# Optimization experiments

Hardware: AMD Instinct MI355X
Metric: run time of the kernel (lower is better)

The kernel has to match this reference:

```python
import jax, jax.numpy as jnp
import numpy as np

B, T, D, H, E, K = 4, 2048, 1024, 2048, 8, 2
LN_EPS = 1e-5


def setup_inputs() -> dict:
    key = jax.random.key(0)
    ks = jax.random.split(key, 5)
    sc = 0.02  # init scale for weights
    return {
        "x": jax.random.normal(ks[0], (B, T, D), dtype=jnp.float32),
        "gate_W": jax.random.normal(ks[1], (D, E), dtype=jnp.float32) * sc,
        "gate_b": jnp.zeros((E,), dtype=jnp.float32),
        "W1": jax.random.normal(ks[2], (E, D, H), dtype=jnp.float32) * sc,
        "b1": jnp.zeros((E, H), dtype=jnp.float32),
        "W2": jax.random.normal(ks[3], (E, H, D), dtype=jnp.float32) * sc,
        "b2": jnp.zeros((E, D), dtype=jnp.float32),
        "ln_gamma": jnp.ones((D,), dtype=jnp.float32),
        "ln_beta": jnp.zeros((D,), dtype=jnp.float32),
    }


def reference(x, gate_W, gate_b, W1, b1, W2, b2, ln_gamma, ln_beta):
    b, t, d = x.shape
    tokens = x.reshape(b * t, d)                      # [N, D]
    n = tokens.shape[0]

    # --- noisy top-k router (eval mode: no noise) ---
    logits = tokens @ gate_W + gate_b                 # [N, E]
    topk_val, topk_idx = jax.lax.top_k(logits, K)     # [N, K]
    topk_prob = jax.nn.softmax(topk_val, axis=-1)
    gates = jnp.zeros_like(logits).at[jnp.arange(n)[:, None], topk_idx].set(topk_prob)  # [N, E]

    # --- experts: dense-equivalent of gather-MLP-scatter (gates are 0 for unselected) ---
    h = jax.nn.gelu(jnp.einsum('nd,edh->enh', tokens, W1) + b1[:, None, :], approximate=False)  # [E,N,H]
    y = jnp.einsum('enh,ehd->end', h, W2) + b2[:, None, :]                                      # [E,N,D]
    out = jnp.einsum('ne,end->nd', gates, y).reshape(b, t, d)

    # --- residual + layernorm ---
    z = out + x
    mu = jnp.mean(z, axis=-1, keepdims=True)
    var = jnp.var(z, axis=-1, keepdims=True)
    out = (z - mu) * jax.lax.rsqrt(var + LN_EPS) * ln_gamma + ln_beta

    # --- aux losses ---
    route_probs = jax.nn.softmax(logits, axis=-1)     # [N, E]
    importance = route_probs.mean(axis=0)             # [E]
    load = (gates > 0).astype(jnp.float32).mean(axis=0)  # [E]
    balance_loss = E * jnp.sum(importance * load)
    eps = 1e-8
    entropy = -(route_probs * jnp.log(route_probs + eps)).sum(axis=-1).mean()
    utilization_entropy = -(load * jnp.log(load + eps)).sum()
    return out, balance_loss, entropy, utilization_entropy, load, importance
```

## Files before the change

### kernel.cpp

```cpp
#include <hip/hip_runtime.h>
#include <math.h>

#define N_TOK 8192
#define DIM   1024
#define HID   2048
#define NE    8
#define NPAIR (N_TOK * 2)
#define CAPP  (NPAIR + NE * 128)
#define TAIL  (N_TOK * DIM)

typedef __bf16 bf16x8_t __attribute__((ext_vector_type(8)));
typedef float  f32x4_t  __attribute__((ext_vector_type(4)));

__device__ __forceinline__ unsigned short f2bf(float f) {
  union { float f; unsigned u; } v; v.f = f;
  unsigned r = v.u + 0x7fffu + ((v.u >> 16) & 1u);
  return (unsigned short)(r >> 16);
}

__device__ __forceinline__ float bf2f(unsigned short h) {
  union { unsigned u; float f; } v; v.u = ((unsigned)h) << 16;
  return v.f;
}

__device__ __forceinline__ float gelu_exact(float v) {
  return 0.5f * v * (1.f + erff(v * 0.70710678118654752440f));
}

__device__ __forceinline__ void load16_lds(const void* g, void* l) {
  __builtin_amdgcn_global_load_lds(
      (const __attribute__((address_space(1))) unsigned int*)g,
      (__attribute__((address_space(3))) unsigned int*)l, 16, 0, 0);
}


template<int KD, int RR>
__device__ __forceinline__ void w2f_body(const float* __restrict__ src,
                                         unsigned short* __restrict__ dst,
                                         int bx, int kblk, int z,
                                         unsigned short (*L)[34], int t) {
  constexpr int KD32 = KD / 32;
  int r0 = bx << 8;
  const float* s = src + (size_t)z * KD * RR + (size_t)(kblk * 32) * RR + r0 + t;
  #pragma unroll
  for (int kk = 0; kk < 32; ++kk)
    L[t][kk] = f2bf(s[(size_t)kk * RR]);
  __syncthreads();
  int lane = t & 63, m16 = lane & 15, q = lane >> 4;
  unsigned short* d = dst + (size_t)z * KD * RR;
  #pragma unroll
  for (int p = 0; p < 4; ++p) {
    int ci = p * 4 + (t >> 6);
    int c = ((r0 >> 4) + ci) * KD32 + kblk;
    uint4 v = *(const uint4*)&L[ci * 16 + m16][q * 8];
    *(uint4*)(d + (size_t)c * 512 + lane * 8) = v;
  }
}

__global__ __launch_bounds__(256) void w_to_frag_all(
    const float* __restrict__ W1, const float* __restrict__ W2,
    unsigned short* __restrict__ W1f, unsigned short* __restrict__ W2f,
    float* __restrict__ stats) {
  __shared__ unsigned short L[256][34];
  int t = threadIdx.x;
  int f = blockIdx.x;
  if (f == 0 && t < 64) stats[t] = 0.f;
  if (f < 2048) {
    int z = f >> 8, r = f & 255;
    w2f_body<DIM, HID>(W1, W1f, r & 7, r >> 3, z, L, t);
  } else {
    int f2 = f - 2048;
    int z = f2 >> 8, r = f2 & 255;
    w2f_body<HID, DIM>(W2, W2f, r & 3, r >> 2, z, L, t);
  }
}

#define R_BLOCKS 512
#define R_TPW    (N_TOK / (R_BLOCKS * 4))
__global__ __launch_bounds__(256) void router_kernel(
    const float* __restrict__ x, const float* __restrict__ gW, const float* __restrict__ gb,
    int* __restrict__ tok_e, float* __restrict__ tok_g,
    int* __restrict__ cnt, float* __restrict__ imp, float* __restrict__ ent_sum) {
  __shared__ int s_cnt[NE];
  __shared__ float s_imp[NE];
  __shared__ float s_ent;
  int tid = threadIdx.x;
  if (tid < NE) { s_cnt[tid] = 0; s_imp[tid] = 0.f; }
  if (tid == 0) s_ent = 0.f;
  __syncthreads();
  int wid = tid >> 6, lane = tid & 63;
  int t0 = (blockIdx.x * 4 + wid) * R_TPW;
  float imp_loc[8] = {0.f, 0.f, 0.f, 0.f, 0.f, 0.f, 0.f, 0.f};
  float ent_loc = 0.f;
  for (int t = 0; t < R_TPW; ++t) {
    int n = t0 + t;
    const float* xr = x + (size_t)n * DIM;
    float p[8] = {0.f, 0.f, 0.f, 0.f, 0.f, 0.f, 0.f, 0.f};
    #pragma unroll
    for (int it = 0; it < DIM / 64; ++it) {
      int d = lane + (it << 6);
      float xv = xr[d];
      const float4* g4 = (const float4*)(gW + (size_t)d * NE);
      float4 a = g4[0], b = g4[1];
      p[0] += xv * a.x; p[1] += xv * a.y; p[2] += xv * a.z; p[3] += xv * a.w;
      p[4] += xv * b.x; p[5] += xv * b.y; p[6] += xv * b.z; p[7] += xv * b.w;
    }
    #pragma unroll
    for (int e = 0; e < 8; ++e)
      for (int o = 32; o > 0; o >>= 1) p[e] += __shfl_down(p[e], o, 64);
    if (lane == 0) {
      float lg[8];
      #pragma unroll
      for (int e = 0; e < 8; ++e) lg[e] = p[e] + gb[e];
      int i0 = 0;
      #pragma unroll
      for (int e = 1; e < 8; ++e) if (lg[e] > lg[i0]) i0 = e;
      int i1 = (i0 == 0) ? 1 : 0;
      #pragma unroll
      for (int e = 0; e < 8; ++e) if (e != i0 && lg[e] > lg[i1]) i1 = e;
      float d1 = expf(lg[i1] - lg[i0]);
      float g0 = 1.f / (1.f + d1);
      float g1 = d1 * g0;
      tok_e[2 * n] = i0; tok_e[2 * n + 1] = i1;
      tok_g[2 * n] = g0; tok_g[2 * n + 1] = g1;
      atomicAdd(&s_cnt[i0], 1);
      atomicAdd(&s_cnt[i1], 1);
      float mx = lg[i0], s = 0.f, pe[8];
      #pragma unroll
      for (int e = 0; e < 8; ++e) { pe[e] = expf(lg[e] - mx); s += pe[e]; }
      float inv = 1.f / s;
      #pragma unroll
      for (int e = 0; e < 8; ++e) {
        float pr = pe[e] * inv;
        imp_loc[e] += pr;
        ent_loc -= pr * logf(pr + 1e-8f);
      }
    }
  }
  if (lane == 0) {
    #pragma unroll
    for (int e = 0; e < 8; ++e) atomicAdd(&s_imp[e], imp_loc[e]);
    atomicAdd(&s_ent, ent_loc);
  }
  __syncthreads();
  const float invN = 1.f / (float)N_TOK;
  if (tid < NE) {
    atomicAdd(&cnt[tid], s_cnt[tid]);
    atomicAdd(&imp[tid], s_imp[tid] * invN);
  }
  if (tid == NE) atomicAdd(ent_sum, s_ent * invN);
}

__global__ __launch_bounds__(256) void scatter_kernel(
    const int* __restrict__ tok_e, const float* __restrict__ tok_g,
    const int* __restrict__ cnt, const float* __restrict__ imp,
    const float* __restrict__ ent_sum,
    int* __restrict__ cursor, int* __restrict__ poffs_g, float* __restrict__ out_tail,
    int* __restrict__ row_token, float* __restrict__ row_gate,
    int* __restrict__ pair_slot) {
  __shared__ int s_cnt[NE], s_base[NE], s_rank[NE];
  int tid = threadIdx.x;
  if (tid < NE) { s_cnt[tid] = 0; s_rank[tid] = 0; }
  __syncthreads();
  int n = blockIdx.x * 256 + tid;
  int e0 = tok_e[2 * n], e1 = tok_e[2 * n + 1];
  atomicAdd(&s_cnt[e0], 1);
  atomicAdd(&s_cnt[e1], 1);
  __syncthreads();
  if (tid < NE) {
    int po = 0;
    for (int e = 0; e < tid; ++e) po += ((cnt[e] + 127) >> 7) << 7;
    s_base[tid] = po + atomicAdd(&cursor[tid], s_cnt[tid]);
  }
  __syncthreads();
  int r0 = atomicAdd(&s_rank[e0], 1);
  int s0 = s_base[e0] + r0;
  row_token[s0] = n; row_gate[s0] = tok_g[2 * n]; pair_slot[2 * n] = s0;
  int r1 = atomicAdd(&s_rank[e1], 1);
  int s1 = s_base[e1] + r1;
  row_token[s1] = n; row_gate[s1] = tok_g[2 * n + 1]; pair_slot[2 * n + 1] = s1;
  if (blockIdx.x == 0 && tid == 0) {
    int off = 0; float bal = 0.f, util = 0.f;
    for (int e = 0; e < NE; ++e) {
      poffs_g[e] = off;
      off += ((cnt[e] + 127) >> 7) << 7;
      float ld = (float)cnt[e] * (1.f / (float)N_TOK);
      float im = imp[e];
      out_tail[3 + e] = ld;
      out_tail[11 + e] = im;
      bal += im * ld;
      util -= ld * logf(ld + 1e-8f);
    }
    poffs_g[NE] = off;
    out_tail[0] = (float)NE * bal;
    out_tail[1] = *ent_sum;
    out_tail[2] = util;
  }
}

#define GA_BLOCKS ((CAPP >> 4) * 32 / 4)
__global__ __launch_bounds__(256) void gather_a1(
    const float* __restrict__ x, const int* __restrict__ row_token,
    const int* __restrict__ cnt, const int* __restrict__ poffs,
    unsigned short* __restrict__ Ab1) {
  int po[NE + 1];
  #pragma unroll
  for (int i = 0; i <= NE; ++i) po[i] = poffs[i];
  int nch = (po[NE] >> 4) * 32;
  int cl = blockIdx.x * 4 + (threadIdx.x >> 6);
  if (cl >= nch) return;
  int lane = threadIdx.x & 63, m16 = lane & 15, q = lane >> 4;
  int sb = cl >> 5, kblk = cl & 31;
  int slot = (sb << 4) + m16;
  int e = 0;
  #pragma unroll
  for (int k = 1; k < NE; ++k) e += (po[k] <= slot) ? 1 : 0;
  int sl = slot - po[e];
  int tok = (sl < cnt[e]) ? row_token[slot] : 0;
  int k = kblk * 32 + q * 8;
  const float4* sp = (const float4*)(x + (size_t)tok * DIM + k);
  float4 v0 = sp[0], v1 = sp[1];
  unsigned short t[8] = {f2bf(v0.x), f2bf(v0.y), f2bf(v0.z), f2bf(v0.w),
                         f2bf(v1.x), f2bf(v1.y), f2bf(v1.z), f2bf(v1.w)};
  *(uint4*)(Ab1 + ((size_t)sb * 32 + kblk) * 512 + lane * 8) = *(uint4*)t;
}

#define GEMM_BLOCKS 1024

__device__ __forceinline__ int xcd_swz(int bid) {
  return (bid & 7) * (GEMM_BLOCKS >> 3) + (bid >> 3);
}

__global__ __launch_bounds__(256, 4) void expert_gemm1(
    const unsigned short* __restrict__ Ab1,
    const unsigned short* __restrict__ W1f,
    const float* __restrict__ b1,
    const int* __restrict__ poffs,
    unsigned short* __restrict__ He) {
  __shared__ __align__(16) unsigned short As[8192], Bs[8192];
  __shared__ int s_po[NE + 1];
  int tid = threadIdx.x, wid = tid >> 6, lane = tid & 63;
  if (tid <= NE) s_po[tid] = poffs[tid];
  __syncthreads();
  int nt = (s_po[NE] >> 7) << 4;
  int m16 = lane & 15, q = lane >> 4;
  int wr = (wid & 1) << 6, wc = (wid >> 1) << 6;
  int ra = wr >> 4, rc = wc >> 4;
  unsigned short* lA = As + wid * 4 * 512;
  unsigned short* lB = Bs + wid * 4 * 512;
  f32x4_t zero4 = {0.f, 0.f, 0.f, 0.f};
  int bid0 = xcd_swz(blockIdx.x);

  for (int tile = bid0; tile < nt; tile += GEMM_BLOCKS) {
    int rt = tile >> 4, ct = tile & 15;
    int col0 = ct << 7;
    int row0 = rt << 7;
    int e = 0;
    while (e + 1 < NE && s_po[e + 1] <= row0) ++e;
    const unsigned short* Ag = Ab1 + ((size_t)((rt << 3) + wid * 2) * 32) * 512 + lane * 8;
    const unsigned short* Bg = W1f + (size_t)e * HID * DIM
                             + ((size_t)((col0 >> 4) + wid * 2) * 32) * 512 + lane * 8;
    f32x4_t acc[4][4];
    #pragma unroll
    for (int i = 0; i < 4; ++i)
      #pragma unroll
      for (int j = 0; j < 4; ++j) acc[i][j] = zero4;

    for (int k0 = 0; k0 < DIM; k0 += 64) {
      int kc = (k0 >> 5) * 512;
      load16_lds(Ag + kc,                  lA);
      load16_lds(Ag + kc + 512,            lA + 512);
      load16_lds(Ag + kc + 32 * 512,       lA + 1024);
      load16_lds(Ag + kc + 32 * 512 + 512, lA + 1536);
      load16_lds(Bg + kc,                  lB);
      load16_lds(Bg + kc + 512,            lB + 512);
      load16_lds(Bg + kc + 32 * 512,       lB + 1024);
      load16_lds(Bg + kc + 32 * 512 + 512, lB + 1536);
      __syncthreads();
      #pragma unroll
      for (int ks = 0; ks < 2; ++ks) {
        bf16x8_t a[4], b[4];
        #pragma unroll
        for (int i = 0; i < 4; ++i) {
          a[i] = *(const bf16x8_t*)&As[((ra + i) * 2 + ks) * 512 + lane * 8];
          b[i] = *(const bf16x8_t*)&Bs[((rc + i) * 2 + ks) * 512 + lane * 8];
        }
        #pragma unroll
        for (int i = 0; i < 4; ++i)
          #pragma unroll
          for (int j = 0; j < 4; ++j)
            acc[i][j] = __builtin_amdgcn_mfma_f32_16x16x32_bf16(a[i], b[j], acc[i][j], 0, 0, 0);
      }
      __syncthreads();
    }

    const float* b1e = b1 + (size_t)e * HID;
    int sb = rt << 3;
    #pragma unroll
    for (int i = 0; i < 4; ++i) {
      size_t sblk = (size_t)(sb + ra + i);
      #pragma unroll
      for (int rr = 0; rr < 4; ++rr) {
        int s15 = q * 4 + rr;
        #pragma unroll
        for (int j = 0; j < 4; ++j) {
          int col = col0 + wc + j * 16 + m16;
          float v = acc[i][j][rr] + b1e[col];
          size_t off = (sblk * 64 + (col >> 5)) * 512 + (((col >> 3) & 3) * 16 + s15) * 8 + (col & 7);
          He[off] = f2bf(gelu_exact(v));
        }
      }
    }
  }
}

__global__ __launch_bounds__(256, 4) void expert_gemm2(
    const unsigned short* __restrict__ He,
    const unsigned short* __restrict__ W2f,
    const int* __restrict__ poffs,
    unsigned short* __restrict__ yb) {
  __shared__ __align__(16) unsigned short As[8192], Bs[8192];
  __shared__ int s_po[NE + 1];
  int tid = threadIdx.x, wid = tid >> 6, lane = tid & 63;
  if (tid <= NE) s_po[tid] = poffs[tid];
  __syncthreads();
  int nt = (s_po[NE] >> 7) << 3;
  int m16 = lane & 15, q = lane >> 4;
  int wr = (wid & 1) << 6, wc = (wid >> 1) << 6;
  int ra = wr >> 4, rc = wc >> 4;
  unsigned short* lA = As + wid * 4 * 512;
  unsigned short* lB = Bs + wid * 4 * 512;
  f32x4_t zero4 = {0.f, 0.f, 0.f, 0.f};
  int bid0 = xcd_swz(blockIdx.x);

  for (int tile = bid0; tile < nt; tile += GEMM_BLOCKS) {
    int rt = tile >> 3, ct = tile & 7;
    int row0 = rt << 7;
    int col0 = ct << 7;
    int e = 0;
    while (e + 1 < NE && s_po[e + 1] <= row0) ++e;
    const unsigned short* Ag = He + ((size_t)((rt << 3) + wid * 2) * 64) * 512 + lane * 8;
    const unsigned short* Bg = W2f + (size_t)e * DIM * HID
                             + ((size_t)((col0 >> 4) + wid * 2) * 64) * 512 + lane * 8;
    f32x4_t acc[4][4];
    #pragma unroll
    for (int i = 0; i < 4; ++i)
      #pragma unroll
      for (int j = 0; j < 4; ++j) acc[i][j] = zero4;

    for (int k0 = 0; k0 < HID; k0 += 64) {
      int kc = (k0 >> 5) * 512;
      load16_lds(Ag + kc,                  lA);
      load16_lds(Ag + kc + 512,            lA + 512);
      load16_lds(Ag + kc + 64 * 512,       lA + 1024);
      load16_lds(Ag + kc + 64 * 512 + 512, lA + 1536);
      load16_lds(Bg + kc,                  lB);
      load16_lds(Bg + kc + 512,            lB + 512);
      load16_lds(Bg + kc + 64 * 512,       lB + 1024);
      load16_lds(Bg + kc + 64 * 512 + 512, lB + 1536);
      __syncthreads();
      #pragma unroll
      for (int ks = 0; ks < 2; ++ks) {
        bf16x8_t a[4], b[4];
        #pragma unroll
        for (int i = 0; i < 4; ++i) {
          a[i] = *(const bf16x8_t*)&As[((ra + i) * 2 + ks) * 512 + lane * 8];
          b[i] = *(const bf16x8_t*)&Bs[((rc + i) * 2 + ks) * 512 + lane * 8];
        }
        #pragma unroll
        for (int i = 0; i < 4; ++i)
          #pragma unroll
          for (int j = 0; j < 4; ++j)
            acc[i][j] = __builtin_amdgcn_mfma_f32_16x16x32_bf16(a[i], b[j], acc[i][j], 0, 0, 0);
      }
      __syncthreads();
    }

    #pragma unroll
    for (int i = 0; i < 4; ++i) {
      #pragma unroll
      for (int rr = 0; rr < 4; ++rr) {
        size_t slot = (size_t)(row0 + wr + i * 16 + q * 4 + rr);
        #pragma unroll
        for (int j = 0; j < 4; ++j) {
          int col = col0 + wc + j * 16 + m16;
          yb[slot * DIM + col] = f2bf(acc[i][j][rr]);
        }
      }
    }
  }
}

__global__ __launch_bounds__(256) void ln_kernel(
    const float* __restrict__ x, const unsigned short* __restrict__ yb,
    const int* __restrict__ tok_e, const float* __restrict__ tok_g,
    const int* __restrict__ pair_slot, const float* __restrict__ b2,
    const float* __restrict__ gamma, const float* __restrict__ beta,
    float* __restrict__ out) {
  int n = blockIdx.x, tid = threadIdx.x;
  int e0 = tok_e[2 * n], e1 = tok_e[2 * n + 1];
  float g0 = tok_g[2 * n], g1 = tok_g[2 * n + 1];
  size_t s0 = (size_t)pair_slot[2 * n], s1 = (size_t)pair_slot[2 * n + 1];
  const float* xr = x + (size_t)n * DIM;
  const unsigned short* y0 = yb + s0 * DIM;
  const unsigned short* y1 = yb + s1 * DIM;
  const float* b2e0 = b2 + (size_t)e0 * DIM;
  const float* b2e1 = b2 + (size_t)e1 * DIM;
  int d0 = tid << 2;
  float4 xv  = *(const float4*)(xr + d0);
  ushort4 yv0 = *(const ushort4*)(y0 + d0);
  ushort4 yv1 = *(const ushort4*)(y1 + d0);
  float4 bv0 = *(const float4*)(b2e0 + d0);
  float4 bv1 = *(const float4*)(b2e1 + d0);
  float z[4], s = 0.f, s2 = 0.f;
  {
    const float* xp = (const float*)&xv;
    const unsigned short* y0p = (const unsigned short*)&yv0;
    const unsigned short* y1p = (const unsigned short*)&yv1;
    const float* b0p = (const float*)&bv0;
    const float* b1p = (const float*)&bv1;
    #pragma unroll
    for (int jj = 0; jj < 4; ++jj) {
      float v = xp[jj] + g0 * (bf2f(y0p[jj]) + b0p[jj]) + g1 * (bf2f(y1p[jj]) + b1p[jj]);
      z[jj] = v; s += v; s2 += v * v;
    }
  }
  for (int o = 32; o > 0; o >>= 1) { s += __shfl_down(s, o, 64); s2 += __shfl_down(s2, o, 64); }
  __shared__ float rs[4], rs2[4];
  int wid = tid >> 6, lane = tid & 63;
  if (lane == 0) { rs[wid] = s; rs2[wid] = s2; }
  __syncthreads();
  float ts = rs[0] + rs[1] + rs[2] + rs[3];
  float ts2 = rs2[0] + rs2[1] + rs2[2] + rs2[3];
  float mu = ts * (1.f / DIM);
  float var = ts2 * (1.f / DIM) - mu * mu;
  float rstd = rsqrtf(var + 1e-5f);
  float4 gv = *(const float4*)(gamma + d0);
  float4 bv = *(const float4*)(beta + d0);
  float4 ov;
  {
    const float* gp = (const float*)&gv;
    const float* bp = (const float*)&bv;
    float* op = (float*)&ov;
    #pragma unroll
    for (int jj = 0; jj < 4; ++jj)
      op[jj] = (z[jj] - mu) * rstd * gp[jj] + bp[jj];
  }
  *(float4*)(out + (size_t)n * DIM + d0) = ov;
}

extern "C" void kernel_launch(void* const* d_in, const int* in_sizes, int n_in,
                              void* d_out, int out_size, void* d_ws, size_t ws_size,
                              hipStream_t stream) {
  const float* x     = (const float*)d_in[0];
  const float* gW    = (const float*)d_in[1];
  const float* gb    = (const float*)d_in[2];
  const float* W1    = (const float*)d_in[3];
  const float* b1    = (const float*)d_in[4];
  const float* W2    = (const float*)d_in[5];
  const float* b2    = (const float*)d_in[6];
  const float* gamma = (const float*)d_in[7];
  const float* beta  = (const float*)d_in[8];
  float* out = (float*)d_out;

  char* w = (char*)d_ws;
  unsigned short* W1f = (unsigned short*)w; w += (size_t)NE * HID * DIM * 2;
  unsigned short* W2f = (unsigned short*)w; w += (size_t)NE * DIM * HID * 2;
  unsigned short* He  = (unsigned short*)w; w += (size_t)CAPP * HID * 2;
  unsigned short* AbY = (unsigned short*)w; w += (size_t)CAPP * DIM * 2;
  int*   row_token    = (int*)w;            w += (size_t)CAPP * 4;
  float* row_gate     = (float*)w;          w += (size_t)CAPP * 4;
  int*   tok_e        = (int*)w;            w += (size_t)NPAIR * 4;
  float* tok_g        = (float*)w;          w += (size_t)NPAIR * 4;
  int*   pair_slot    = (int*)w;            w += (size_t)NPAIR * 4;
  float* imp          = (float*)w;
  float* ent_sum      = imp + 8;
  int*   cntp         = (int*)(imp + 16);
  int*   cursor       = cntp + 8;
  int*   poffs        = cursor + 8;

  unsigned short* Ab1 = AbY;
  unsigned short* yb  = AbY;

  w_to_frag_all<<<4096, 256, 0, stream>>>(W1, W2, W1f, W2f, imp);
  router_kernel<<<R_BLOCKS, 256, 0, stream>>>(x, gW, gb, tok_e, tok_g, cntp, imp, ent_sum);
  scatter_kernel<<<N_TOK / 256, 256, 0, stream>>>(tok_e, tok_g, cntp, imp, ent_sum,
                                                  cursor, poffs, out + TAIL,
                                                  row_token, row_gate, pair_slot);
  gather_a1<<<GA_BLOCKS, 256, 0, stream>>>(x, row_token, cntp, poffs, Ab1);
  expert_gemm1<<<GEMM_BLOCKS, 256, 0, stream>>>(Ab1, W1f, b1, poffs, He);
  expert_gemm2<<<GEMM_BLOCKS, 256, 0, stream>>>(He, W2f, poffs, yb);
  ln_kernel<<<N_TOK, 256, 0, stream>>>(x, yb, tok_e, tok_g, pair_slot, b2, gamma, beta, out);
}
```

Before: 451.6 us.

## Fuse router into weight-prep kernel and use contiguous tile ranges in GEMMs

Merges the weight-to-fragment conversion and the router into one launch, so router blocks run alongside the weight conversion blocks and one kernel launch is dropped. Global atomics for counts, importance and entropy are replaced by per-block partials that each scatter block reduces itself, which removes the need to zero stats before the router. Both expert GEMMs now give each block a contiguous range of tiles (assuming 1024 blocks) instead of a strided loop, which improves locality of shared weight columns and rows. Costs include a redundant partial reduction in every scatter block and possible load imbalance from the range split.

```diff
diff --git a/kernel.cpp b/kernel.cpp
--- a/kernel.cpp
+++ b/kernel.cpp
@@ -33,6 +33,10 @@
       (__attribute__((address_space(3))) unsigned int*)l, 16, 0, 0);
 }
 
+
+#define W2F_BLOCKS 4096
+#define R_BLOCKS   512
+#define R_TPW      (N_TOK / (R_BLOCKS * 4))
 
 template<int KD, int RR>
 __device__ __forceinline__ void w2f_body(const float* __restrict__ src,
@@ -57,43 +61,43 @@
   }
 }
 
-__global__ __launch_bounds__(256) void w_to_frag_all(
+__global__ __launch_bounds__(256) void prep_kernel(
     const float* __restrict__ W1, const float* __restrict__ W2,
     unsigned short* __restrict__ W1f, unsigned short* __restrict__ W2f,
-    float* __restrict__ stats) {
+    const float* __restrict__ x, const float* __restrict__ gW, const float* __restrict__ gb,
+    int* __restrict__ tok_e, float* __restrict__ tok_g,
+    int* __restrict__ pcnt,
+    float* __restrict__ pimp,
+    float* __restrict__ pent,
+    int* __restrict__ cursor) {
   __shared__ unsigned short L[256][34];
+  __shared__ int s_cnt[NE];
+  __shared__ float s_imp[NE];
+  __shared__ float s_ent;
   int t = threadIdx.x;
   int f = blockIdx.x;
-  if (f == 0 && t < 64) stats[t] = 0.f;
   if (f < 2048) {
     int z = f >> 8, r = f & 255;
     w2f_body<DIM, HID>(W1, W1f, r & 7, r >> 3, z, L, t);
-  } else {
+    return;
+  }
+  if (f < W2F_BLOCKS) {
     int f2 = f - 2048;
     int z = f2 >> 8, r = f2 & 255;
     w2f_body<HID, DIM>(W2, W2f, r & 3, r >> 2, z, L, t);
-  }
-}
-
-#define R_BLOCKS 512
-#define R_TPW    (N_TOK / (R_BLOCKS * 4))
-__global__ __launch_bounds__(256) void router_kernel(
-    const float* __restrict__ x, const float* __restrict__ gW, const float* __restrict__ gb,
-    int* __restrict__ tok_e, float* __restrict__ tok_g,
-    int* __restrict__ cnt, float* __restrict__ imp, float* __restrict__ ent_sum) {
-  __shared__ int s_cnt[NE];
-  __shared__ float s_imp[NE];
-  __shared__ float s_ent;
-  int tid = threadIdx.x;
-  if (tid < NE) { s_cnt[tid] = 0; s_imp[tid] = 0.f; }
-  if (tid == 0) s_ent = 0.f;
-  __syncthreads();
-  int wid = tid >> 6, lane = tid & 63;
-  int t0 = (blockIdx.x * 4 + wid) * R_TPW;
+    return;
+  }
+  int rb = f - W2F_BLOCKS;
+  if (rb == 0 && t < NE) cursor[t] = 0;
+  if (t < NE) { s_cnt[t] = 0; s_imp[t] = 0.f; }
+  if (t == 0) s_ent = 0.f;
+  __syncthreads();
+  int wid = t >> 6, lane = t & 63;
+  int t0 = (rb * 4 + wid) * R_TPW;
   float imp_loc[8] = {0.f, 0.f, 0.f, 0.f, 0.f, 0.f, 0.f, 0.f};
   float ent_loc = 0.f;
-  for (int t = 0; t < R_TPW; ++t) {
-    int n = t0 + t;
+  for (int tt = 0; tt < R_TPW; ++tt) {
+    int n = t0 + tt;
     const float* xr = x + (size_t)n * DIM;
     float p[8] = {0.f, 0.f, 0.f, 0.f, 0.f, 0.f, 0.f, 0.f};
     #pragma unroll
@@ -143,25 +147,41 @@
     atomicAdd(&s_ent, ent_loc);
   }
   __syncthreads();
-  const float invN = 1.f / (float)N_TOK;
-  if (tid < NE) {
-    atomicAdd(&cnt[tid], s_cnt[tid]);
-    atomicAdd(&imp[tid], s_imp[tid] * invN);
-  }
-  if (tid == NE) atomicAdd(ent_sum, s_ent * invN);
+  if (t < NE) { pcnt[rb * NE + t] = s_cnt[t]; pimp[rb * NE + t] = s_imp[t]; }
+  if (t == NE) pent[rb] = s_ent;
 }
 
 __global__ __launch_bounds__(256) void scatter_kernel(
     const int* __restrict__ tok_e, const float* __restrict__ tok_g,
-    const int* __restrict__ cnt, const float* __restrict__ imp,
-    const float* __restrict__ ent_sum,
-    int* __restrict__ cursor, int* __restrict__ poffs_g, float* __restrict__ out_tail,
+    const int* __restrict__ pcnt, const float* __restrict__ pimp,
+    const float* __restrict__ pent,
+    int* __restrict__ cursor, int* __restrict__ poffs_g, int* __restrict__ cnt_out,
+    float* __restrict__ out_tail,
     int* __restrict__ row_token, float* __restrict__ row_gate,
     int* __restrict__ pair_slot) {
   __shared__ int s_cnt[NE], s_base[NE], s_rank[NE];
+  __shared__ int g_cnt[NE];
+  __shared__ float g_imp[NE], g_ent;
   int tid = threadIdx.x;
-  if (tid < NE) { s_cnt[tid] = 0; s_rank[tid] = 0; }
-  __syncthreads();
+  if (tid < NE) { s_cnt[tid] = 0; s_rank[tid] = 0; g_cnt[tid] = 0; g_imp[tid] = 0.f; }
+  if (tid == 0) g_ent = 0.f;
+  __syncthreads();
+  {
+    int e = tid & 7, rg = tid >> 3;
+    int acc = 0;
+    #pragma unroll
+    for (int r = 0; r < 16; ++r) acc += pcnt[(rg * 16 + r) * NE + e];
+    atomicAdd(&g_cnt[e], acc);
+  }
+  if (blockIdx.x == 0) {
+    int e = tid & 7, rg = tid >> 3;
+    float fa = 0.f;
+    #pragma unroll
+    for (int r = 0; r < 16; ++r) fa += pimp[(rg * 16 + r) * NE + e];
+    atomicAdd(&g_imp[e], fa);
+    float ea = pent[tid] + pent[tid + 256];
+    atomicAdd(&g_ent, ea);
+  }
   int n = blockIdx.x * 256 + tid;
   int e0 = tok_e[2 * n], e1 = tok_e[2 * n + 1];
   atomicAdd(&s_cnt[e0], 1);
@@ -169,7 +189,7 @@
   __syncthreads();
   if (tid < NE) {
     int po = 0;
-    for (int e = 0; e < tid; ++e) po += ((cnt[e] + 127) >> 7) << 7;
+    for (int e = 0; e < tid; ++e) po += ((g_cnt[e] + 127) >> 7) << 7;
     s_base[tid] = po + atomicAdd(&cursor[tid], s_cnt[tid]);
   }
   __syncthreads();
@@ -180,12 +200,14 @@
   int s1 = s_base[e1] + r1;
   row_token[s1] = n; row_gate[s1] = tok_g[2 * n + 1]; pair_slot[2 * n + 1] = s1;
   if (blockIdx.x == 0 && tid == 0) {
+    const float invN = 1.f / (float)N_TOK;
     int off = 0; float bal = 0.f, util = 0.f;
     for (int e = 0; e < NE; ++e) {
       poffs_g[e] = off;
-      off += ((cnt[e] + 127) >> 7) << 7;
-      float ld = (float)cnt[e] * (1.f / (float)N_TOK);
-      float im = imp[e];
+      cnt_out[e] = g_cnt[e];
+      off += ((g_cnt[e] + 127) >> 7) << 7;
+      float ld = (float)g_cnt[e] * invN;
+      float im = g_imp[e] * invN;
       out_tail[3 + e] = ld;
       out_tail[11 + e] = im;
       bal += im * ld;
@@ -193,7 +215,7 @@
     }
     poffs_g[NE] = off;
     out_tail[0] = (float)NE * bal;
-    out_tail[1] = *ent_sum;
+    out_tail[1] = g_ent * invN;
     out_tail[2] = util;
   }
 }
@@ -249,9 +271,11 @@
   unsigned short* lA = As + wid * 4 * 512;
   unsigned short* lB = Bs + wid * 4 * 512;
   f32x4_t zero4 = {0.f, 0.f, 0.f, 0.f};
-  int bid0 = xcd_swz(blockIdx.x);
-
-  for (int tile = bid0; tile < nt; tile += GEMM_BLOCKS) {
+  int swz = xcd_swz(blockIdx.x);
+  int lo = (int)(((long long)swz * nt) >> 10);
+  int hi = (int)(((long long)(swz + 1) * nt) >> 10);
+
+  for (int tile = lo; tile < hi; ++tile) {
     int rt = tile >> 4, ct = tile & 15;
     int col0 = ct << 7;
     int row0 = rt << 7;
@@ -331,9 +355,11 @@
   unsigned short* lA = As + wid * 4 * 512;
   unsigned short* lB = Bs + wid * 4 * 512;
   f32x4_t zero4 = {0.f, 0.f, 0.f, 0.f};
-  int bid0 = xcd_swz(blockIdx.x);
-
-  for (int tile = bid0; tile < nt; tile += GEMM_BLOCKS) {
+  int swz = xcd_swz(blockIdx.x);
+  int lo = (int)(((long long)swz * nt) >> 10);
+  int hi = (int)(((long long)(swz + 1) * nt) >> 10);
+
+  for (int tile = lo; tile < hi; ++tile) {
     int rt = tile >> 3, ct = tile & 7;
     int row0 = rt << 7;
     int col0 = ct << 7;
@@ -473,21 +499,22 @@
   int*   tok_e        = (int*)w;            w += (size_t)NPAIR * 4;
   float* tok_g        = (float*)w;          w += (size_t)NPAIR * 4;
   int*   pair_slot    = (int*)w;            w += (size_t)NPAIR * 4;
-  float* imp          = (float*)w;
-  float* ent_sum      = imp + 8;
-  int*   cntp         = (int*)(imp + 16);
-  int*   cursor       = cntp + 8;
-  int*   poffs        = cursor + 8;
+  int*   cursor       = (int*)w;            w += 64;
+  int*   poffs        = (int*)w;            w += 64;
+  int*   cnt_out      = (int*)w;            w += 64;
+  int*   pcnt         = (int*)w;            w += (size_t)R_BLOCKS * NE * 4;
+  float* pimp         = (float*)w;          w += (size_t)R_BLOCKS * NE * 4;
+  float* pent         = (float*)w;          w += (size_t)R_BLOCKS * 4;
 
   unsigned short* Ab1 = AbY;
   unsigned short* yb  = AbY;
 
-  w_to_frag_all<<<4096, 256, 0, stream>>>(W1, W2, W1f, W2f, imp);
-  router_kernel<<<R_BLOCKS, 256, 0, stream>>>(x, gW, gb, tok_e, tok_g, cntp, imp, ent_sum);
-  scatter_kernel<<<N_TOK / 256, 256, 0, stream>>>(tok_e, tok_g, cntp, imp, ent_sum,
-                                                  cursor, poffs, out + TAIL,
-                                                  row_token, row_gate, pair_slot);
-  gather_a1<<<GA_BLOCKS, 256, 0, stream>>>(x, row_token, cntp, poffs, Ab1);
+  prep_kernel<<<W2F_BLOCKS + R_BLOCKS, 256, 0, stream>>>(
+      W1, W2, W1f, W2f, x, gW, gb, tok_e, tok_g, pcnt, pimp, pent, cursor);
+  scatter_kernel<<<N_TOK / 256, 256, 0, stream>>>(
+      tok_e, tok_g, pcnt, pimp, pent, cursor, poffs, cnt_out, out + TAIL,
+      row_token, row_gate, pair_slot);
+  gather_a1<<<GA_BLOCKS, 256, 0, stream>>>(x, row_token, cnt_out, poffs, Ab1);
   expert_gemm1<<<GEMM_BLOCKS, 256, 0, stream>>>(Ab1, W1f, b1, poffs, He);
   expert_gemm2<<<GEMM_BLOCKS, 256, 0, stream>>>(He, W2f, poffs, yb);
   ln_kernel<<<N_TOK, 256, 0, stream>>>(x, yb, tok_e, tok_g, pair_slot, b2, gamma, beta, out);
```

Result: slower. 495.7 us (+9.8%).
